# Kernel tuning notes

Hardware: AMD Instinct MI355X
Metric: run time of the kernel (lower is better)

The kernel has to match this reference:

```python
import jax, jax.numpy as jnp
import numpy as np

E = 1024
H = 16
D = E // H  # head dim 64


def setup_inputs() -> dict:
    key = jax.random.key(0)
    ks = jax.random.split(key, 6)
    s = E ** -0.5
    return {
        "x": jax.random.normal(ks[0], (2, 2048, E), dtype=jnp.float32),
        "Wq": jax.random.normal(ks[1], (E, E), dtype=jnp.float32) * s,
        "Wk": jax.random.normal(ks[2], (E, E), dtype=jnp.float32) * s,
        "Wv": jax.random.normal(ks[3], (E, E), dtype=jnp.float32) * s,
        "Wo": jax.random.normal(ks[4], (E, E), dtype=jnp.float32) * s,
        "bo": jax.random.normal(ks[5], (E,), dtype=jnp.float32) * 0.01,
    }


def reference(x, Wq, Wk, Wv, Wo, bo):
    B, T, _ = x.shape
    # per-head bias-free projections, batched as one GEMM each then split heads
    q = (x @ Wq).reshape(B, T, H, D)
    k = (x @ Wk).reshape(B, T, H, D)
    v = (x @ Wv).reshape(B, T, H, D)
    scores = jnp.einsum("bqhd,bkhd->bhqk", q, k) * (D ** -0.5)
    causal = jnp.tril(jnp.ones((T, T), dtype=bool))
    scores = jnp.where(causal, scores, -jnp.inf)
    attn = jax.nn.softmax(scores, axis=-1)  # dropout p=0 (eval)
    out = jnp.einsum("bhqk,bkhd->bqhd", attn, v).reshape(B, T, E)
    return out @ Wo + bo
```

## Files before the change

kernel.cpp:

```cpp
#include <hip/hip_runtime.h>
#include <hip/hip_bf16.h>
#include <stdint.h>

typedef __hip_bfloat16 bf16;
typedef __attribute__((ext_vector_type(8))) short bf16x8;
typedef __attribute__((ext_vector_type(4))) float f32x4;
typedef __attribute__((ext_vector_type(16))) float f32x16;

#define MFMA16(a,b,c) __builtin_amdgcn_mfma_f32_16x16x32_bf16((a),(b),(c),0,0,0)
#define MFMA32(a,b,c) __builtin_amdgcn_mfma_f32_32x32x16_bf16((a),(b),(c),0,0,0)

#define B_ 2
#define T_ 2048
#define E_ 1024
#define H_ 16
#define D_ 64
#define M_ (B_*T_)
#define PROJ_ELEMS (32ull * 2048ull * 64ull)

__device__ __forceinline__ void gload_lds16(const bf16* g, bf16* l) {
  __builtin_amdgcn_global_load_lds(
      (const __attribute__((address_space(1))) unsigned int*)g,
      (__attribute__((address_space(3))) unsigned int*)l,
      16, 0, 0);
}

__global__ __launch_bounds__(256) void cvt_x_kernel(const float* __restrict__ in,
                                                    bf16* __restrict__ out) {
  int i = blockIdx.x * 256 + threadIdx.x;
  float4 v = reinterpret_cast<const float4*>(in)[i];
  union { bf16 h[4]; unsigned long long u; } t;
  t.h[0] = __float2bfloat16(v.x);
  t.h[1] = __float2bfloat16(v.y);
  t.h[2] = __float2bfloat16(v.z);
  t.h[3] = __float2bfloat16(v.w);
  reinterpret_cast<unsigned long long*>(out)[i] = t.u;
}

__global__ __launch_bounds__(256) void transpose_cvt4_kernel(
    const float* __restrict__ W0, const float* __restrict__ W1,
    const float* __restrict__ W2, const float* __restrict__ W3,
    bf16* __restrict__ T0, bf16* __restrict__ T1,
    bf16* __restrict__ T2, bf16* __restrict__ T3) {
  __shared__ float tile[32][33];
  const float* W; bf16* Wt;
  switch (blockIdx.z) {
    case 0: W = W0; Wt = T0; break;
    case 1: W = W1; Wt = T1; break;
    case 2: W = W2; Wt = T2; break;
    default: W = W3; Wt = T3; break;
  }
  const int tx = threadIdx.x, ty = threadIdx.y;
  const int n0 = blockIdx.x * 32, k0 = blockIdx.y * 32;
#pragma unroll
  for (int i = 0; i < 4; i++)
    tile[ty + 8*i][tx] = W[(size_t)(k0 + ty + 8*i) * E_ + n0 + tx];
  __syncthreads();
#pragma unroll
  for (int i = 0; i < 4; i++)
    Wt[(size_t)(n0 + ty + 8*i) * E_ + k0 + tx] = __float2bfloat16(tile[tx][ty + 8*i]);
}

__global__ __launch_bounds__(256) void gemm_bt_kernel(
    const bf16* __restrict__ A, const bf16* __restrict__ Bt,
    void* __restrict__ out, const float* __restrict__ bias,
    const int mode, const float scale)
{
  constexpr int K = E_;
  __shared__ __align__(16) bf16 As[128*32];
  __shared__ __align__(16) bf16 Bs[128*32];
  const int tid = threadIdx.x;
  const int w = tid >> 6, l = tid & 63;
  const int lc = l & 15, lr = l >> 4;
  const int m0 = blockIdx.y * 128, n0 = blockIdx.x * 128;
  const int wr = (w >> 1) * 64, wc = (w & 1) * 64;

  f32x4 acc[4][4];
#pragma unroll
  for (int m = 0; m < 4; m++)
#pragma unroll
    for (int n = 0; n < 4; n++) acc[m][n] = (f32x4)0.0f;

  const int srow = l >> 2;
  const int scol = (l & 3) * 8;

  for (int k0 = 0; k0 < K; k0 += 32) {
#pragma unroll
    for (int p = 0; p < 2; p++) {
      const int r = (w*2 + p) * 16 + srow;
      gload_lds16(A  + (size_t)(m0 + r) * K + k0 + scol, &As[(w*2 + p) * 512]);
      gload_lds16(Bt + (size_t)(n0 + r) * K + k0 + scol, &Bs[(w*2 + p) * 512]);
    }
    __syncthreads();
    bf16x8 af[4], bfr[4];
#pragma unroll
    for (int m = 0; m < 4; m++)
      af[m] = *reinterpret_cast<const bf16x8*>(&As[(wr + m*16 + lc) * 32 + lr * 8]);
#pragma unroll
    for (int n = 0; n < 4; n++)
      bfr[n] = *reinterpret_cast<const bf16x8*>(&Bs[(wc + n*16 + lc) * 32 + lr * 8]);
#pragma unroll
    for (int m = 0; m < 4; m++)
#pragma unroll
      for (int n = 0; n < 4; n++)
        acc[m][n] = MFMA16(af[m], bfr[n], acc[m][n]);
    __syncthreads();
  }

  const int proj = blockIdx.x >> 3;
#pragma unroll
  for (int m = 0; m < 4; m++) {
#pragma unroll
    for (int n = 0; n < 4; n++) {
#pragma unroll
      for (int j = 0; j < 4; j++) {
        const int row = m0 + wr + m*16 + lr*4 + j;
        const int col = n0 + wc + n*16 + lc;
        if (mode == 2) {
          reinterpret_cast<float*>(out)[(size_t)row * E_ + col] = acc[m][n][j] + bias[col];
        } else {
          const int cp = col & (E_-1);
          const int b = row >> 11, t = row & (T_-1);
          const int h = cp >> 6,  d = cp & (D_-1);
          const float v = acc[m][n][j] * (proj == 0 ? scale : 1.0f);
          size_t idx;
          if (proj == 2) idx = (((size_t)(b*H_ + h)) * D_ + d) * T_ + t;
          else           idx = (((size_t)(b*H_ + h)) * T_ + t) * D_ + d;
          reinterpret_cast<bf16*>(out)[proj * PROJ_ELEMS + idx] = __float2bfloat16(v);
        }
      }
    }
  }
}

__global__ __launch_bounds__(128, 2) void attn_fwd_kernel(
    const bf16* __restrict__ Q, const bf16* __restrict__ Kt,
    const bf16* __restrict__ Vt, bf16* __restrict__ O)
{
  const int tid = threadIdx.x;
  const int w = tid >> 6, l = tid & 63;
  const int ln = l & 31;
  const int hi = l >> 5;
  const int bid = blockIdx.x;
  const int bh  = (bid & 7) * 4 + ((bid >> 3) & 3);
  const int p   = bid >> 5;
  const int qt  = w ? p : 63 - p;
  const int q0  = qt * 32;

  const bf16* Qb = Q  + (size_t)bh * T_ * D_;
  const bf16* kp = Kt + (size_t)bh * T_ * D_ + (size_t)ln * D_ + hi*8;
  const bf16* vp = Vt + (size_t)bh * D_ * T_ + (size_t)ln * T_ + hi*8;

  bf16x8 qf[4];
#pragma unroll
  for (int s = 0; s < 4; s++)
    qf[s] = *reinterpret_cast<const bf16x8*>(
        &Qb[(size_t)(q0 + ln) * D_ + s*16 + hi*8]);

  f32x16 oacc0 = (f32x16)0.0f, oacc1 = (f32x16)0.0f;
  float mrow = -1e30f, psum = 0.0f;

  bf16x8 kA[4], vA[2][2], kB[4], vB[2][2];

#define LOADKV(KK, VV, KT) do {                                              \
    _Pragma("unroll")                                                        \
    for (int s_ = 0; s_ < 4; s_++)                                           \
      KK[s_] = *reinterpret_cast<const bf16x8*>(                             \
          kp + (size_t)(KT)*32*D_ + s_*16);                                  \
    _Pragma("unroll")                                                        \
    for (int a_ = 0; a_ < 2; a_++)                                           \
      _Pragma("unroll")                                                      \
      for (int s_ = 0; s_ < 2; s_++)                                         \
        VV[a_][s_] = *reinterpret_cast<const bf16x8*>(                       \
            vp + (size_t)a_*32*T_ + (KT)*32 + s_*16);                        \
  } while (0)

  union U4 { uint32_t u[4]; bf16x8 v; };
  union PK { bf16 h[2]; uint32_t u; };

#define TILE_BODY(KK, VV, KKN, VVN, KT, PRE, MASK) do {                      \
    if (PRE) { LOADKV(KKN, VVN, (KT)+1); }                                   \
    f32x16 sT = (f32x16)0.0f;                                                \
    _Pragma("unroll")                                                        \
    for (int s_ = 0; s_ < 4; s_++) sT = MFMA32(KK[s_], qf[s_], sT);          \
    if (MASK) {                                                              \
      _Pragma("unroll")                                                      \
      for (int r_ = 0; r_ < 16; r_++) {                                      \
        const int mm = (r_&3) + 8*(r_>>2) + 4*hi;                            \
        if (mm > ln) sT[r_] = -1e30f;                                        \
      }                                                                      \
    }                                                                        \
    float tmax = fmaxf(fmaxf(fmaxf(sT[0],sT[1]), fmaxf(sT[2],sT[3])),        \
                       fmaxf(fmaxf(sT[4],sT[5]), fmaxf(sT[6],sT[7])));       \
    tmax = fmaxf(tmax,                                                       \
           fmaxf(fmaxf(fmaxf(sT[8],sT[9]),  fmaxf(sT[10],sT[11])),           \
                 fmaxf(fmaxf(sT[12],sT[13]),fmaxf(sT[14],sT[15]))));         \
    tmax = fmaxf(tmax, __shfl_xor(tmax, 32));                                \
    const float mn_ = fmaxf(mrow, tmax);                                     \
    const float fsc = exp2f(mrow - mn_);                                     \
    mrow = mn_;                                                              \
    psum *= fsc;                                                             \
    _Pragma("unroll")                                                        \
    for (int r_ = 0; r_ < 16; r_++) {                                        \
      const float pe = exp2f(sT[r_] - mn_);                                  \
      sT[r_] = pe;                                                           \
      psum += pe;                                                            \
    }                                                                        \
    oacc0 *= fsc;                                                            \
    oacc1 *= fsc;                                                            \
    uint32_t u_[8];                                                          \
    _Pragma("unroll")                                                        \
    for (int i_ = 0; i_ < 8; i_++) {                                         \
      PK pk_;                                                                \
      pk_.h[0] = __float2bfloat16(sT[2*i_]);                                 \
      pk_.h[1] = __float2bfloat16(sT[2*i_+1]);                               \
      u_[i_] = pk_.u;                                                        \
    }                                                                        \
    const uint32_t x0 = __shfl_xor(hi ? u_[0] : u_[2], 32);                  \
    const uint32_t x1 = __shfl_xor(hi ? u_[1] : u_[3], 32);                  \
    const uint32_t x2 = __shfl_xor(hi ? u_[4] : u_[6], 32);                  \
    const uint32_t x3 = __shfl_xor(hi ? u_[5] : u_[7], 32);                  \
    U4 pf0, pf1;                                                             \
    pf0.u[0] = hi ? x0 : u_[0];  pf0.u[1] = hi ? x1 : u_[1];                 \
    pf0.u[2] = hi ? u_[2] : x0;  pf0.u[3] = hi ? u_[3] : x1;                 \
    pf1.u[0] = hi ? x2 : u_[4];  pf1.u[1] = hi ? x3 : u_[5];                 \
    pf1.u[2] = hi ? u_[6] : x2;  pf1.u[3] = hi ? u_[7] : x3;                 \
    oacc0 = MFMA32(VV[0][0], pf0.v, oacc0);                                  \
    oacc0 = MFMA32(VV[0][1], pf1.v, oacc0);                                  \
    oacc1 = MFMA32(VV[1][0], pf0.v, oacc1);                                  \
    oacc1 = MFMA32(VV[1][1], pf1.v, oacc1);                                  \
  } while (0)

  LOADKV(kA, vA, 0);

  int kt = 0;
  while (kt + 2 <= qt) {
    TILE_BODY(kA, vA, kB, vB, kt,   true, false);
    TILE_BODY(kB, vB, kA, vA, kt+1, true, false);
    kt += 2;
  }
  if (kt < qt) {
    TILE_BODY(kA, vA, kB, vB, kt, true, false);
    TILE_BODY(kB, vB, kA, vA, qt, false, true);
  } else {
    TILE_BODY(kA, vA, kB, vB, qt, false, true);
  }

  psum += __shfl_xor(psum, 32);
  const float inv = 1.0f / psum;
  const int b = bh >> 4, h = bh & 15;
  const size_t rowbase = (size_t)(b * T_ + q0 + ln) * E_ + h * 64;
#pragma unroll
  for (int r = 0; r < 16; r++) {
    const int d = (r&3) + 8*(r>>2) + 4*hi;
    O[rowbase + d] = __float2bfloat16(oacc0[r] * inv);
  }
#pragma unroll
  for (int r = 0; r < 16; r++) {
    const int d = 32 + (r&3) + 8*(r>>2) + 4*hi;
    O[rowbase + d] = __float2bfloat16(oacc1[r] * inv);
  }
#undef TILE_BODY
#undef LOADKV
}

extern "C" void kernel_launch(void* const* d_in, const int* in_sizes, int n_in,
                              void* d_out, int out_size, void* d_ws, size_t ws_size,
                              hipStream_t stream) {
  const float* x  = (const float*)d_in[0];
  const float* Wq = (const float*)d_in[1];
  const float* Wk = (const float*)d_in[2];
  const float* Wv = (const float*)d_in[3];
  const float* Wo = (const float*)d_in[4];
  const float* bo = (const float*)d_in[5];
  float* out = (float*)d_out;

  char* ws = (char*)d_ws;
  bf16* xb  = (bf16*)(ws);
  bf16* WqT = (bf16*)(ws + (8ull  << 20));
  bf16* WkT = (bf16*)(ws + (10ull << 20));
  bf16* WvT = (bf16*)(ws + (12ull << 20));
  bf16* WoT = (bf16*)(ws + (14ull << 20));
  bf16* Qb  = (bf16*)(ws + (16ull << 20));
  bf16* Ob  = (bf16*)(ws + (40ull << 20));

  cvt_x_kernel<<<4096, 256, 0, stream>>>(x, xb);
  transpose_cvt4_kernel<<<dim3(32, 32, 4), dim3(32, 8), 0, stream>>>(
      Wq, Wk, Wv, Wo, WqT, WkT, WvT, WoT);

  const float qscale = 0.125f * 1.44269504f;
  gemm_bt_kernel<<<dim3(24, 32), 256, 0, stream>>>(xb, WqT, Qb, nullptr, 3, qscale);

  attn_fwd_kernel<<<1024, 128, 0, stream>>>(
      Qb, Qb + PROJ_ELEMS, Qb + 2*PROJ_ELEMS, Ob);

  gemm_bt_kernel<<<dim3(8, 32), 256, 0, stream>>>(Ob, WoT, out, bo, 2, 1.0f);
}
```

Measured before the change: 153.8 us.

## Split KV range across waves per query tile and rescale softmax lazily

Each block now owns a single 32-row query tile. The old scheme paired two tiles per block to balance causal work. Now the two waves split that tile's key range in half and merge their partial max, sum and output through shared memory. The grid doubles to 2048 blocks and launch bounds allow 4 blocks per CU, to raise parallelism and shorten the longest per-wave dependency chain. The online-softmax rescale is also skipped unless the running max grows by more than 8 in the log2 domain, which saves exp and scale work but adds an LDS round-trip, a barrier and more register pressure.

```diff
diff --git a/kernel.cpp b/kernel.cpp
--- a/kernel.cpp
+++ b/kernel.cpp
@@ -133,18 +133,21 @@
   }
 }
 
-__global__ __launch_bounds__(128, 2) void attn_fwd_kernel(
+__global__ __launch_bounds__(128, 4) void attn_fwd_kernel(
     const bf16* __restrict__ Q, const bf16* __restrict__ Kt,
     const bf16* __restrict__ Vt, bf16* __restrict__ O)
 {
+  __shared__ float Lm[32];
+  __shared__ float Ll[32];
+  __shared__ float Lo[64 * 33];
+
   const int tid = threadIdx.x;
   const int w = tid >> 6, l = tid & 63;
   const int ln = l & 31;
   const int hi = l >> 5;
   const int bid = blockIdx.x;
   const int bh  = (bid & 7) * 4 + ((bid >> 3) & 3);
-  const int p   = bid >> 5;
-  const int qt  = w ? p : 63 - p;
+  const int qt  = 63 - (bid >> 5);
   const int q0  = qt * 32;
 
   const bf16* Qb = Q  + (size_t)bh * T_ * D_;
@@ -196,18 +199,20 @@
            fmaxf(fmaxf(fmaxf(sT[8],sT[9]),  fmaxf(sT[10],sT[11])),           \
                  fmaxf(fmaxf(sT[12],sT[13]),fmaxf(sT[14],sT[15]))));         \
     tmax = fmaxf(tmax, __shfl_xor(tmax, 32));                                \
-    const float mn_ = fmaxf(mrow, tmax);                                     \
-    const float fsc = exp2f(mrow - mn_);                                     \
-    mrow = mn_;                                                              \
-    psum *= fsc;                                                             \
+    if (!__all(tmax <= mrow + 8.0f)) {                                       \
+      const float mn_ = fmaxf(mrow, tmax);                                   \
+      const float fsc = exp2f(mrow - mn_);                                   \
+      mrow = mn_;                                                            \
+      psum *= fsc;                                                           \
+      oacc0 *= fsc;                                                          \
+      oacc1 *= fsc;                                                          \
+    }                                                                        \
     _Pragma("unroll")                                                        \
     for (int r_ = 0; r_ < 16; r_++) {                                        \
-      const float pe = exp2f(sT[r_] - mn_);                                  \
+      const float pe = exp2f(sT[r_] - mrow);                                 \
       sT[r_] = pe;                                                           \
       psum += pe;                                                            \
     }                                                                        \
-    oacc0 *= fsc;                                                            \
-    oacc1 *= fsc;                                                            \
     uint32_t u_[8];                                                          \
     _Pragma("unroll")                                                        \
     for (int i_ = 0; i_ < 8; i_++) {                                         \
@@ -231,34 +236,57 @@
     oacc1 = MFMA32(VV[1][1], pf1.v, oacc1);                                  \
   } while (0)
 
-  LOADKV(kA, vA, 0);
-
-  int kt = 0;
-  while (kt + 2 <= qt) {
-    TILE_BODY(kA, vA, kB, vB, kt,   true, false);
-    TILE_BODY(kB, vB, kA, vA, kt+1, true, false);
-    kt += 2;
-  }
-  if (kt < qt) {
-    TILE_BODY(kA, vA, kB, vB, kt, true, false);
-    TILE_BODY(kB, vB, kA, vA, qt, false, true);
-  } else {
-    TILE_BODY(kA, vA, kB, vB, qt, false, true);
+  const int nkt = qt + 1;
+  const int h = nkt >> 1;
+  const int kt_lo = w ? h : 0;
+  const int kt_hi = w ? nkt : h;
+
+  if (kt_lo < kt_hi) {
+    LOADKV(kA, vA, kt_lo);
+    int kt = kt_lo;
+    while (kt + 2 <= kt_hi) {
+      TILE_BODY(kA, vA, kB, vB, kt, true, false);
+      if (kt + 2 == kt_hi) {
+        if (kt + 1 == qt) TILE_BODY(kB, vB, kA, vA, kt+1, false, true);
+        else              TILE_BODY(kB, vB, kA, vA, kt+1, false, false);
+      } else {
+        TILE_BODY(kB, vB, kA, vA, kt+1, true, false);
+      }
+      kt += 2;
+    }
+    if (kt < kt_hi) {
+      if (kt == qt) TILE_BODY(kA, vA, kB, vB, kt, false, true);
+      else          TILE_BODY(kA, vA, kB, vB, kt, false, false);
+    }
   }
 
   psum += __shfl_xor(psum, 32);
-  const float inv = 1.0f / psum;
-  const int b = bh >> 4, h = bh & 15;
-  const size_t rowbase = (size_t)(b * T_ + q0 + ln) * E_ + h * 64;
-#pragma unroll
-  for (int r = 0; r < 16; r++) {
-    const int d = (r&3) + 8*(r>>2) + 4*hi;
-    O[rowbase + d] = __float2bfloat16(oacc0[r] * inv);
-  }
-#pragma unroll
-  for (int r = 0; r < 16; r++) {
-    const int d = 32 + (r&3) + 8*(r>>2) + 4*hi;
-    O[rowbase + d] = __float2bfloat16(oacc1[r] * inv);
+
+  if (w == 1) {
+    if (hi == 0) { Lm[ln] = mrow; Ll[ln] = psum; }
+#pragma unroll
+    for (int r = 0; r < 16; r++) {
+      const int d = (r&3) + 8*(r>>2) + 4*hi;
+      Lo[d * 33 + ln] = oacc0[r];
+      Lo[(32 + d) * 33 + ln] = oacc1[r];
+    }
+  }
+  __syncthreads();
+
+  if (w == 0) {
+    const float m1 = Lm[ln], l1 = Ll[ln];
+    const float mn = fmaxf(mrow, m1);
+    const float f0 = exp2f(mrow - mn);
+    const float f1 = exp2f(m1 - mn);
+    const float inv = 1.0f / (psum * f0 + l1 * f1);
+    const int b = bh >> 4, hh = bh & 15;
+    const size_t rowbase = (size_t)(b * T_ + q0 + ln) * E_ + hh * 64;
+#pragma unroll
+    for (int r = 0; r < 16; r++) {
+      const int d = (r&3) + 8*(r>>2) + 4*hi;
+      O[rowbase + d]      = __float2bfloat16((oacc0[r]*f0 + Lo[d*33 + ln]*f1) * inv);
+      O[rowbase + 32 + d] = __float2bfloat16((oacc1[r]*f0 + Lo[(32+d)*33 + ln]*f1) * inv);
+    }
   }
 #undef TILE_BODY
 #undef LOADKV
@@ -291,7 +319,7 @@
   const float qscale = 0.125f * 1.44269504f;
   gemm_bt_kernel<<<dim3(24, 32), 256, 0, stream>>>(xb, WqT, Qb, nullptr, 3, qscale);
 
-  attn_fwd_kernel<<<1024, 128, 0, stream>>>(
+  attn_fwd_kernel<<<2048, 128, 0, stream>>>(
       Qb, Qb + PROJ_ELEMS, Qb + 2*PROJ_ELEMS, Ob);
 
   gemm_bt_kernel<<<dim3(8, 32), 256, 0, stream>>>(Ob, WoT, out, bo, 2, 1.0f);
```

New measurement: 195.0 us. 26.8% more time.

## Share K/V tiles across four waves via swizzled LDS double buffering

Applied to the files above, without the earlier changes.

The attention kernel moves from 2-wave blocks that each read K/V straight from global memory into registers to 4-wave blocks covering 128 consecutive query rows. These blocks cooperatively stage each 32-key K/V tile into XOR-swizzled, double-buffered shared memory with global_load_lds, so every tile is read from global once per block instead of once per wave. It also adds a lazy rescale that skips the max update and accumulator rescale while the new tile max stays within 8 of the running max. The cost is a block-wide barrier per tile, idle waves on tiles past their causal limit, and the loss of the old pairing of short and long query tiles for load balance.

```diff
diff --git a/kernel.cpp b/kernel.cpp
--- a/kernel.cpp
+++ b/kernel.cpp
@@ -133,23 +133,28 @@
   }
 }
 
-__global__ __launch_bounds__(128, 2) void attn_fwd_kernel(
+__global__ __launch_bounds__(256, 2) void attn_fwd_kernel(
     const bf16* __restrict__ Q, const bf16* __restrict__ Kt,
     const bf16* __restrict__ Vt, bf16* __restrict__ O)
 {
+  __shared__ __align__(16) bf16 Ks[2][32 * 64];
+  __shared__ __align__(16) bf16 Vs[2][64 * 32];
+
   const int tid = threadIdx.x;
   const int w = tid >> 6, l = tid & 63;
   const int ln = l & 31;
   const int hi = l >> 5;
   const int bid = blockIdx.x;
   const int bh  = (bid & 7) * 4 + ((bid >> 3) & 3);
-  const int p   = bid >> 5;
-  const int qt  = w ? p : 63 - p;
-  const int q0  = qt * 32;
+  const int qb  = 15 - (bid >> 5);
+  const int q0  = qb * 128 + w * 32;
 
   const bf16* Qb = Q  + (size_t)bh * T_ * D_;
-  const bf16* kp = Kt + (size_t)bh * T_ * D_ + (size_t)ln * D_ + hi*8;
-  const bf16* vp = Vt + (size_t)bh * D_ * T_ + (size_t)ln * T_ + hi*8;
+  const bf16* Kb = Kt + (size_t)bh * T_ * D_;
+  const bf16* Vb = Vt + (size_t)bh * D_ * T_;
+
+  const bf16* ksrc = Kb + (size_t)(w*8 + (l>>3)) * D_ + (((l&7) ^ (l>>3)) << 3);
+  const bf16* vsrc = Vb + (size_t)(w*16 + (l>>2)) * T_ + (((l&3) ^ ((l>>2)&3)) << 3);
 
   bf16x8 qf[4];
 #pragma unroll
@@ -160,90 +165,99 @@
   f32x16 oacc0 = (f32x16)0.0f, oacc1 = (f32x16)0.0f;
   float mrow = -1e30f, psum = 0.0f;
 
-  bf16x8 kA[4], vA[2][2], kB[4], vB[2][2];
-
-#define LOADKV(KK, VV, KT) do {                                              \
-    _Pragma("unroll")                                                        \
-    for (int s_ = 0; s_ < 4; s_++)                                           \
-      KK[s_] = *reinterpret_cast<const bf16x8*>(                             \
-          kp + (size_t)(KT)*32*D_ + s_*16);                                  \
-    _Pragma("unroll")                                                        \
-    for (int a_ = 0; a_ < 2; a_++)                                           \
-      _Pragma("unroll")                                                      \
-      for (int s_ = 0; s_ < 2; s_++)                                         \
-        VV[a_][s_] = *reinterpret_cast<const bf16x8*>(                       \
-            vp + (size_t)a_*32*T_ + (KT)*32 + s_*16);                        \
-  } while (0)
-
   union U4 { uint32_t u[4]; bf16x8 v; };
   union PK { bf16 h[2]; uint32_t u; };
 
-#define TILE_BODY(KK, VV, KKN, VVN, KT, PRE, MASK) do {                      \
-    if (PRE) { LOADKV(KKN, VVN, (KT)+1); }                                   \
-    f32x16 sT = (f32x16)0.0f;                                                \
-    _Pragma("unroll")                                                        \
-    for (int s_ = 0; s_ < 4; s_++) sT = MFMA32(KK[s_], qf[s_], sT);          \
-    if (MASK) {                                                              \
-      _Pragma("unroll")                                                      \
-      for (int r_ = 0; r_ < 16; r_++) {                                      \
-        const int mm = (r_&3) + 8*(r_>>2) + 4*hi;                            \
-        if (mm > ln) sT[r_] = -1e30f;                                        \
-      }                                                                      \
-    }                                                                        \
-    float tmax = fmaxf(fmaxf(fmaxf(sT[0],sT[1]), fmaxf(sT[2],sT[3])),        \
-                       fmaxf(fmaxf(sT[4],sT[5]), fmaxf(sT[6],sT[7])));       \
-    tmax = fmaxf(tmax,                                                       \
-           fmaxf(fmaxf(fmaxf(sT[8],sT[9]),  fmaxf(sT[10],sT[11])),           \
-                 fmaxf(fmaxf(sT[12],sT[13]),fmaxf(sT[14],sT[15]))));         \
-    tmax = fmaxf(tmax, __shfl_xor(tmax, 32));                                \
-    const float mn_ = fmaxf(mrow, tmax);                                     \
-    const float fsc = exp2f(mrow - mn_);                                     \
-    mrow = mn_;                                                              \
-    psum *= fsc;                                                             \
-    _Pragma("unroll")                                                        \
-    for (int r_ = 0; r_ < 16; r_++) {                                        \
-      const float pe = exp2f(sT[r_] - mn_);                                  \
-      sT[r_] = pe;                                                           \
-      psum += pe;                                                            \
-    }                                                                        \
-    oacc0 *= fsc;                                                            \
-    oacc1 *= fsc;                                                            \
-    uint32_t u_[8];                                                          \
-    _Pragma("unroll")                                                        \
-    for (int i_ = 0; i_ < 8; i_++) {                                         \
-      PK pk_;                                                                \
-      pk_.h[0] = __float2bfloat16(sT[2*i_]);                                 \
-      pk_.h[1] = __float2bfloat16(sT[2*i_+1]);                               \
-      u_[i_] = pk_.u;                                                        \
-    }                                                                        \
-    const uint32_t x0 = __shfl_xor(hi ? u_[0] : u_[2], 32);                  \
-    const uint32_t x1 = __shfl_xor(hi ? u_[1] : u_[3], 32);                  \
-    const uint32_t x2 = __shfl_xor(hi ? u_[4] : u_[6], 32);                  \
-    const uint32_t x3 = __shfl_xor(hi ? u_[5] : u_[7], 32);                  \
-    U4 pf0, pf1;                                                             \
-    pf0.u[0] = hi ? x0 : u_[0];  pf0.u[1] = hi ? x1 : u_[1];                 \
-    pf0.u[2] = hi ? u_[2] : x0;  pf0.u[3] = hi ? u_[3] : x1;                 \
-    pf1.u[0] = hi ? x2 : u_[4];  pf1.u[1] = hi ? x3 : u_[5];                 \
-    pf1.u[2] = hi ? u_[6] : x2;  pf1.u[3] = hi ? u_[7] : x3;                 \
-    oacc0 = MFMA32(VV[0][0], pf0.v, oacc0);                                  \
-    oacc0 = MFMA32(VV[0][1], pf1.v, oacc0);                                  \
-    oacc1 = MFMA32(VV[1][0], pf0.v, oacc1);                                  \
-    oacc1 = MFMA32(VV[1][1], pf1.v, oacc1);                                  \
-  } while (0)
-
-  LOADKV(kA, vA, 0);
-
-  int kt = 0;
-  while (kt + 2 <= qt) {
-    TILE_BODY(kA, vA, kB, vB, kt,   true, false);
-    TILE_BODY(kB, vB, kA, vA, kt+1, true, false);
-    kt += 2;
-  }
-  if (kt < qt) {
-    TILE_BODY(kA, vA, kB, vB, kt, true, false);
-    TILE_BODY(kB, vB, kA, vA, qt, false, true);
-  } else {
-    TILE_BODY(kA, vA, kB, vB, qt, false, true);
+  const int my_last = 4*qb + w;
+  const int nkt = 4*qb + 4;
+
+  gload_lds16(ksrc, &Ks[0][w << 9]);
+  gload_lds16(vsrc, &Vs[0][w << 9]);
+  __syncthreads();
+
+  for (int kt = 0; kt < nkt; ++kt) {
+    const int buf = kt & 1;
+    const int kbase = kt << 5;
+    if (kt + 1 < nkt) {
+      gload_lds16(ksrc + (size_t)(kbase + 32) * D_, &Ks[buf^1][w << 9]);
+      gload_lds16(vsrc + (kbase + 32),              &Vs[buf^1][w << 9]);
+    }
+    if (kt <= my_last) {
+      bf16x8 kf[4];
+#pragma unroll
+      for (int s = 0; s < 4; s++) {
+        const int ch = 2*s + hi;
+        kf[s] = *reinterpret_cast<const bf16x8*>(
+            &Ks[buf][ln*64 + ((ch ^ (ln & 7)) << 3)]);
+      }
+      f32x16 sT = (f32x16)0.0f;
+#pragma unroll
+      for (int s = 0; s < 4; s++) sT = MFMA32(kf[s], qf[s], sT);
+
+      if (kt == my_last) {
+#pragma unroll
+        for (int r = 0; r < 16; r++) {
+          const int mm = (r&3) + 8*(r>>2) + 4*hi;
+          if (mm > ln) sT[r] = -1e30f;
+        }
+      }
+
+      float tmax = fmaxf(fmaxf(fmaxf(sT[0],sT[1]), fmaxf(sT[2],sT[3])),
+                         fmaxf(fmaxf(sT[4],sT[5]), fmaxf(sT[6],sT[7])));
+      tmax = fmaxf(tmax,
+             fmaxf(fmaxf(fmaxf(sT[8],sT[9]),  fmaxf(sT[10],sT[11])),
+                   fmaxf(fmaxf(sT[12],sT[13]),fmaxf(sT[14],sT[15]))));
+      tmax = fmaxf(tmax, __shfl_xor(tmax, 32));
+      if (!__all(tmax <= mrow + 8.0f)) {
+        const float mn_ = fmaxf(mrow, tmax);
+        const float fsc = exp2f(mrow - mn_);
+        mrow = mn_;
+        psum *= fsc;
+        oacc0 *= fsc;
+        oacc1 *= fsc;
+      }
+#pragma unroll
+      for (int r = 0; r < 16; r++) {
+        const float pe = exp2f(sT[r] - mrow);
+        sT[r] = pe;
+        psum += pe;
+      }
+
+      uint32_t u_[8];
+#pragma unroll
+      for (int i = 0; i < 8; i++) {
+        PK pk;
+        pk.h[0] = __float2bfloat16(sT[2*i]);
+        pk.h[1] = __float2bfloat16(sT[2*i+1]);
+        u_[i] = pk.u;
+      }
+      const uint32_t x0 = __shfl_xor(hi ? u_[0] : u_[2], 32);
+      const uint32_t x1 = __shfl_xor(hi ? u_[1] : u_[3], 32);
+      const uint32_t x2 = __shfl_xor(hi ? u_[4] : u_[6], 32);
+      const uint32_t x3 = __shfl_xor(hi ? u_[5] : u_[7], 32);
+      U4 pf0, pf1;
+      pf0.u[0] = hi ? x0 : u_[0];  pf0.u[1] = hi ? x1 : u_[1];
+      pf0.u[2] = hi ? u_[2] : x0;  pf0.u[3] = hi ? u_[3] : x1;
+      pf1.u[0] = hi ? x2 : u_[4];  pf1.u[1] = hi ? x3 : u_[5];
+      pf1.u[2] = hi ? u_[6] : x2;  pf1.u[3] = hi ? u_[7] : x3;
+
+#pragma unroll
+      for (int a = 0; a < 2; a++) {
+        const int r0 = a*32 + ln;
+        bf16x8 vf0 = *reinterpret_cast<const bf16x8*>(
+            &Vs[buf][r0*32 + (((0 + hi) ^ (r0 & 3)) << 3)]);
+        bf16x8 vf1 = *reinterpret_cast<const bf16x8*>(
+            &Vs[buf][r0*32 + (((2 + hi) ^ (r0 & 3)) << 3)]);
+        if (a == 0) {
+          oacc0 = MFMA32(vf0, pf0.v, oacc0);
+          oacc0 = MFMA32(vf1, pf1.v, oacc0);
+        } else {
+          oacc1 = MFMA32(vf0, pf0.v, oacc1);
+          oacc1 = MFMA32(vf1, pf1.v, oacc1);
+        }
+      }
+    }
+    __syncthreads();
   }
 
   psum += __shfl_xor(psum, 32);
@@ -260,8 +274,6 @@
     const int d = 32 + (r&3) + 8*(r>>2) + 4*hi;
     O[rowbase + d] = __float2bfloat16(oacc1[r] * inv);
   }
-#undef TILE_BODY
-#undef LOADKV
 }
 
 extern "C" void kernel_launch(void* const* d_in, const int* in_sizes, int n_in,
@@ -291,7 +303,7 @@
   const float qscale = 0.125f * 1.44269504f;
   gemm_bt_kernel<<<dim3(24, 32), 256, 0, stream>>>(xb, WqT, Qb, nullptr, 3, qscale);
 
-  attn_fwd_kernel<<<1024, 128, 0, stream>>>(
+  attn_fwd_kernel<<<512, 256, 0, stream>>>(
       Qb, Qb + PROJ_ELEMS, Qb + 2*PROJ_ELEMS, Ob);
 
   gemm_bt_kernel<<<dim3(8, 32), 256, 0, stream>>>(Ob, WoT, out, bo, 2, 1.0f);
```

New measurement: 160.5 us. 4.4% more time.
